# Optimization experiments

Measured on AMD Instinct MI355X. Metric: run time of the kernel, lower is better.

The kernel has to match this reference:

```python
import jax, jax.numpy as jnp
import numpy as np

N = 50_000       # nodes
E = 1_600_000    # edges (avg degree 32)
D = 32           # emb_dim == hidden_dim, num_heads = 1
L = 8            # num_layers
K = 8            # SortPooling k
VOCAB = 100


def setup_inputs() -> dict:
    key = jax.random.key(0)
    ks = jax.random.split(key, 20)
    def nrm(k, shape, scale=0.1):
        return jax.random.normal(k, shape, dtype=jnp.float32) * scale
    return {
        "h_tok": jax.random.randint(ks[0], (N,), 0, VOCAB),
        "e_tok": jax.random.randint(ks[1], (E,), 0, VOCAB),
        "src": jax.random.randint(ks[2], (E,), 0, N),
        "dst": jax.random.randint(ks[3], (E,), 0, N),
        "tok_emb": nrm(ks[4], (VOCAB, D)),
        "e_tok_emb": nrm(ks[5], (VOCAB, D)),
        # per-layer EGATConv params (stacked over L layers; all dims are D->D)
        "W_ni": nrm(ks[6], (L, D, D)),
        "W_nj": nrm(ks[7], (L, D, D)),
        "W_fij": nrm(ks[8], (L, D, D)),
        "b_edge": nrm(ks[9], (L, D)),
        "attn": nrm(ks[10], (L, D)),
        "W_node": nrm(ks[11], (L, D, D)),
        # MLP head
        "W_lin": nrm(ks[12], (K * D, D)),
        "b_lin": nrm(ks[13], (D,)),
        "W1": nrm(ks[14], (D, D)),
        "b1": nrm(ks[15], (D,)),
        "W2": nrm(ks[16], (D, D)),
        "b2": nrm(ks[17], (D,)),
        "Wc": nrm(ks[18], (D, 2)),
        "bc": nrm(ks[19], (2,)),
    }


def _egat_layer(h, e, src, dst, Wni, Wnj, Wfij, b, attn, Wnode):
    """DGL EGATConv, num_heads=1. h: [N,D] nodes, e: [E,D] edges."""
    n = h.shape[0]
    # per-edge feature: f_ij = LeakyReLU(A*h_i + B*h_j + C*e_ij + b)
    f = jax.nn.leaky_relu((h @ Wni)[src] + (h @ Wnj)[dst] + e @ Wfij + b, 0.01)  # [E,D]
    logits = jnp.sum(f * attn, axis=-1)                                         # [E]
    # edge softmax over incoming edges of each destination node
    m = jax.ops.segment_max(logits, dst, num_segments=n)
    ex = jnp.exp(logits - m[dst])
    a = ex / jax.ops.segment_sum(ex, dst, num_segments=n)[dst]                  # [E]
    msg = (h @ Wnode)[src] * a[:, None]                                         # [E,D]
    h_out = jax.ops.segment_sum(msg, dst, num_segments=n)                       # [N,D]
    return h_out, f


def reference(h_tok, e_tok, src, dst, tok_emb, e_tok_emb, W_ni, W_nj, W_fij,
              b_edge, attn, W_node, W_lin, b_lin, W1, b1, W2, b2, Wc, bc):
    h = jax.nn.relu(tok_emb[h_tok])   # [N,D]
    e = e_tok_emb[e_tok]              # [E,D]

    def step(carry, p):
        h, e = carry
        Wni, Wnj, Wfij, b, at, Wn = p
        h2, e2 = _egat_layer(h, e, src, dst, Wni, Wnj, Wfij, b, at, Wn)
        return (jax.nn.relu(h2), e2), None

    (h, e), _ = jax.lax.scan(step, (h, e), (W_ni, W_nj, W_fij, b_edge, attn, W_node))

    # SortPooling(k): sort each node's features ascending, rank nodes by last
    # (largest) channel descending, keep top-k nodes, flatten. Single graph.
    hs = jnp.sort(h, axis=-1)                     # [N,D]
    _, idx = jax.lax.top_k(hs[:, -1], K)          # top-k nodes
    x = hs[idx].reshape(1, K * D)                 # [1, k*D]

    x = jax.nn.relu(x @ W_lin + b_lin)
    x = jax.nn.relu(x @ W1 + b1)
    x = jax.nn.relu(x @ W2 + b2)
    return x @ Wc + bc                            # [1, 2]
```

## Files before the change

kernel.cpp:

```cpp
#include <hip/hip_runtime.h>
#include <hip/hip_fp16.h>

#define DD 32
#define NLAYERS 8
#define TOPK 8
#define NPB 256
#define HNB 1024
#define BCH 4096
#define P2CAP 12288

typedef _Float16 half8 __attribute__((ext_vector_type(8)));
typedef float f32x4 __attribute__((ext_vector_type(4)));

__device__ __forceinline__ unsigned encf(float x){ unsigned u=__float_as_uint(x); return (u&0x80000000u)? ~u : (u|0x80000000u); }
__device__ __forceinline__ unsigned short f2h(float f){ return __half_as_ushort(__float2half(f)); }
__device__ __forceinline__ float h2f(unsigned short u){ return __half2float(__ushort_as_half(u)); }
__device__ __forceinline__ float4 up4(uint2 u){
  float4 r;
  r.x=h2f((unsigned short)(u.x&0xFFFFu)); r.y=h2f((unsigned short)(u.x>>16));
  r.z=h2f((unsigned short)(u.y&0xFFFFu)); r.w=h2f((unsigned short)(u.y>>16));
  return r;
}
union HU { uint2 u; half8 h; };
union HU4 { uint4 u; half8 h; };
__device__ __forceinline__ int gidx(const void* p, long i, int i64){
  return i64 ? (int)((const long long*)p)[i] : ((const int*)p)[i];
}

__global__ __launch_bounds__(1024) void k_detect(const int* __restrict__ srcw,
                                                 int* __restrict__ iflag,
                                                 int* __restrict__ bcnt){
  int tid = threadIdx.x;
  for (int i=tid;i<HNB;i+=1024) bcnt[i]=0;
  if (tid==0){
    int allz = 1;
    for (int k=1;k<32;k+=2) if (srcw[k]!=0) allz = 0;
    *iflag = allz;
  }
}

__global__ void k_init(const void* __restrict__ h_tok,
                       const float* __restrict__ tok_emb,
                       unsigned short* __restrict__ h16,
                       const int* __restrict__ iflag, int N)
{
  int i64 = *iflag;
  long idx = (long)blockIdx.x*blockDim.x + threadIdx.x;
  if (idx >= (long)N*8) return;
  int n=(int)(idx>>3), q=(int)(idx&7);
  int t = gidx(h_tok, n, i64);
  float4 v = reinterpret_cast<const float4*>(tok_emb)[t*8+q];
  uint2 o;
  o.x = (unsigned)f2h(fmaxf(v.x,0.f)) | ((unsigned)f2h(fmaxf(v.y,0.f))<<16);
  o.y = (unsigned)f2h(fmaxf(v.z,0.f)) | ((unsigned)f2h(fmaxf(v.w,0.f))<<16);
  reinterpret_cast<uint2*>(h16)[(long)n*8+q] = o;
}

__global__ __launch_bounds__(256) void k_hist(
    const void* __restrict__ dstv, int* __restrict__ bcnt,
    const int* __restrict__ iflag, int E, int NB)
{
  __shared__ int bins[HNB];
  int i64 = *iflag;
  int tid = threadIdx.x;
  for (int i=tid;i<NB;i+=256) bins[i]=0;
  __syncthreads();
  long base = (long)blockIdx.x * BCH;
  long rem = (long)E - base;
  int nloc = (rem < BCH) ? (int)rem : BCH;
  for (int t=tid; t<nloc; t+=256){
    int d = gidx(dstv, base+t, i64);
    atomicAdd(&bins[d>>8], 1);
  }
  __syncthreads();
  for (int i=tid;i<NB;i+=256){
    int v = bins[i];
    if (v) atomicAdd(&bcnt[i], v);
  }
}

__global__ __launch_bounds__(1024) void k_bscan(const int* __restrict__ bcnt,
    int* __restrict__ bbase, int* __restrict__ gcur, int NB, int E)
{
  __shared__ int wsum[16];
  int tid=threadIdx.x, lane=tid&63, w=tid>>6;
  int v = (tid<NB)? bcnt[tid]:0;
  int x=v;
  #pragma unroll
  for (int d=1;d<64;d<<=1){ int t=__shfl_up(x,d,64); if(lane>=d) x+=t; }
  if (lane==63) wsum[w]=x;
  __syncthreads();
  if (w==0 && lane<16){
    int y=wsum[lane];
    #pragma unroll
    for (int d=1;d<16;d<<=1){ int t=__shfl_up(y,d,64); if(lane>=d) y+=t; }
    wsum[lane]=y;
  }
  __syncthreads();
  int wb = (w>0)? wsum[w-1]:0;
  int ex = x - v + wb;
  if (tid<NB){ bbase[tid]=ex; gcur[tid]=ex; }
  if (tid==0) bbase[NB]=E;
}

__global__ __launch_bounds__(256) void k_bucket(
    const void* __restrict__ srcv, const void* __restrict__ dstv,
    int* __restrict__ gcur, uint2* __restrict__ btmp,
    const int* __restrict__ iflag, int E, int NB)
{
  __shared__ int hist[HNB];
  __shared__ int cbase[HNB];
  int i64 = *iflag;
  int tid = threadIdx.x;
  long base = (long)blockIdx.x * BCH;
  long rem = (long)E - base;
  int nloc = (rem < BCH) ? (int)rem : BCH;
  if (nloc <= 0) return;
  for (int i = tid; i < NB; i += 256) hist[i] = 0;
  __syncthreads();
  int dl[BCH/256];
  #pragma unroll
  for (int k = 0; k < BCH/256; k++){
    int t = tid + k*256;
    dl[k] = -1;
    if (t < nloc){
      int d = gidx(dstv, base + t, i64);
      dl[k] = d;
      atomicAdd(&hist[d>>8], 1);
    }
  }
  __syncthreads();
  for (int i = tid; i < NB; i += 256){
    int hv = hist[i];
    cbase[i] = hv ? atomicAdd(&gcur[i], hv) : 0;
    hist[i] = 0;
  }
  __syncthreads();
  #pragma unroll
  for (int k = 0; k < BCH/256; k++){
    int t = tid + k*256;
    if (t < nloc){
      int d = dl[k];
      int s = gidx(srcv, base + t, i64);
      int b = d>>8;
      int slot = cbase[b] + atomicAdd(&hist[b], 1);
      uint2 r; r.x = ((unsigned)d<<16) | (unsigned)s; r.y = (unsigned)(base + t);
      btmp[slot] = r;
    }
  }
}

__global__ __launch_bounds__(256) void k_bsort(
    const int* __restrict__ bbase, const uint2* __restrict__ btmp,
    uint2* __restrict__ sde8, int* __restrict__ off, int N, int NB)
{
  __shared__ int lcnt[NPB];
  __shared__ int lbase[NPB];
  __shared__ int wsum2[4];
  __shared__ uint2 lrec[P2CAP];
  int bkt = blockIdx.x;
  int base = bbase[bkt], endp = bbase[bkt+1];
  int sz = endp - base;
  int lo = bkt*NPB;
  int tid = threadIdx.x;
  lcnt[tid] = 0;
  __syncthreads();
  for (int i=tid;i<sz;i+=256){
    uint2 r = btmp[base+i];
    atomicAdd(&lcnt[(int)(r.x>>16) - lo], 1);
  }
  __syncthreads();
  int v = lcnt[tid];
  int lane = tid&63, w = tid>>6;
  int x = v;
  #pragma unroll
  for (int d=1;d<64;d<<=1){ int t=__shfl_up(x,d,64); if(lane>=d) x+=t; }
  if (lane==63) wsum2[w]=x;
  __syncthreads();
  if (tid==0){ int a=0; for(int i=0;i<4;i++){ int t=wsum2[i]; wsum2[i]=a; a+=t; } }
  __syncthreads();
  int ex = x - v + wsum2[w];
  lbase[tid] = ex;
  int node = lo + tid;
  if (node < N) off[node] = base + ex;
  if (bkt == NB-1 && tid == 0) off[N] = bbase[NB];
  __syncthreads();
  if (sz <= P2CAP){
    lcnt[tid] = lbase[tid];
    __syncthreads();
    for (int i=tid;i<sz;i+=256){
      uint2 r = btmp[base+i];
      int d = (int)(r.x>>16) - lo;
      int p = atomicAdd(&lcnt[d],1);
      lrec[p] = r;
    }
    __syncthreads();
    for (int i=tid;i<sz;i+=256)
      sde8[base+i] = lrec[i];
  } else {
    lcnt[tid] = base + lbase[tid];
    __syncthreads();
    for (int i=tid;i<sz;i+=256){
      uint2 r = btmp[base+i];
      int d = (int)(r.x>>16) - lo;
      int p = atomicAdd(&lcnt[d],1);
      sde8[p] = r;
    }
  }
}

__global__ void k_fill(const uint2* __restrict__ sde8, const void* __restrict__ e_tok,
                       const float* __restrict__ e_emb,
                       unsigned* __restrict__ csr_sd, unsigned short* __restrict__ ebuf,
                       const int* __restrict__ iflag, int E){
  int i64 = *iflag;
  long idx = (long)blockIdx.x*blockDim.x + threadIdx.x;
  if (idx >= (long)E*4) return;
  int pos = (int)(idx>>2), j = (int)(idx&3);
  uint2 r = sde8[pos];
  if (j==0) csr_sd[pos] = r.x;
  int t = gidx(e_tok, (int)r.y, i64);
  const float4* sp = reinterpret_cast<const float4*>(e_emb + t*DD) + j*2;
  float4 x = sp[0], y = sp[1];
  uint4 ov;
  ov.x = (unsigned)f2h(x.x) | ((unsigned)f2h(x.y)<<16);
  ov.y = (unsigned)f2h(x.z) | ((unsigned)f2h(x.w)<<16);
  ov.z = (unsigned)f2h(y.x) | ((unsigned)f2h(y.y)<<16);
  ov.w = (unsigned)f2h(y.z) | ((unsigned)f2h(y.w)<<16);
  reinterpret_cast<uint4*>(ebuf)[(long)pos*4+j] = ov;
}

__global__ __launch_bounds__(256) void k_nodeAB(
    const unsigned short* __restrict__ h16,
    const float* __restrict__ WA, const float* __restrict__ WB,
    unsigned short* __restrict__ hA16, unsigned short* __restrict__ hB16, int N)
{
  __shared__ float hl[8][DD];
  int tid = threadIdx.x;
  int ln = tid>>5, c = tid&31;
  int n = blockIdx.x*8 + ln;
  hl[ln][c] = (n<N)? h2f(h16[(long)n*DD+c]) : 0.f;
  __syncthreads();
  float a=0.f,b=0.f;
  #pragma unroll
  for (int k=0;k<DD;k++){
    float v = hl[ln][k];
    a = fmaf(v, WA[k*DD+c], a);
    b = fmaf(v, WB[k*DD+c], b);
  }
  if (n<N){ hA16[(long)n*DD+c]=f2h(a); hB16[(long)n*DD+c]=f2h(b); }
}

__global__ __launch_bounds__(256) void k_edge(
    unsigned short* __restrict__ ebuf,
    const unsigned short* __restrict__ hA16, const unsigned short* __restrict__ hB16,
    const unsigned* __restrict__ csr_sd,
    const float* __restrict__ Wf, const float* __restrict__ bvec,
    const float* __restrict__ attn,
    unsigned short* __restrict__ lbuf, int ntiles, int writef)
{
  int lane = threadIdx.x & 63;
  int wid = (blockIdx.x*256 + threadIdx.x) >> 6;
  int nw  = (gridDim.x*256) >> 6;
  int m = lane & 15, q = lane >> 4;
  half8 a0, a1;
  #pragma unroll
  for (int j=0;j<8;j++){
    a0[j] = (_Float16)Wf[(q*8+j)*DD + m];
    a1[j] = (_Float16)Wf[(q*8+j)*DD + 16 + m];
  }
  float4 blo = *reinterpret_cast<const float4*>(bvec + q*4);
  float4 bhi = *reinterpret_cast<const float4*>(bvec + 16 + q*4);
  float4 alo = *reinterpret_cast<const float4*>(attn + q*4);
  float4 ahi = *reinterpret_cast<const float4*>(attn + 16 + q*4);
  f32x4 zero = {0.f,0.f,0.f,0.f};
  HU4 b0; b0.u = make_uint4(0,0,0,0);
  HU4 b1; b1.u = make_uint4(0,0,0,0);
  unsigned sd0 = 0, sd1 = 0;
  uint2 gA0_0={0,0}, gA1_0={0,0}, gB0_0={0,0}, gB1_0={0,0};
  if (wid < ntiles){
    long e0 = (long)wid*16 + m;
    sd0 = csr_sd[e0];
    b0.u = *reinterpret_cast<const uint4*>(ebuf + e0*DD + q*8);
    unsigned s = sd0 & 0xFFFFu, d = sd0 >> 16;
    const uint2* pA = reinterpret_cast<const uint2*>(hA16 + (long)s*DD);
    const uint2* pB = reinterpret_cast<const uint2*>(hB16 + (long)d*DD);
    gA0_0=pA[q]; gA1_0=pA[4+q]; gB0_0=pB[q]; gB1_0=pB[4+q];
  }
  if (wid + nw < ntiles){
    long e1 = (long)(wid+nw)*16 + m;
    sd1 = csr_sd[e1];
    b1.u = *reinterpret_cast<const uint4*>(ebuf + e1*DD + q*8);
  }
  for (int t = wid; t < ntiles; t += nw){
    int t1 = t + nw, t2 = t + 2*nw;
    unsigned sd2 = 0; HU4 b2; b2.u = make_uint4(0,0,0,0);
    if (t2 < ntiles){
      long e2 = (long)t2*16 + m;
      sd2 = csr_sd[e2];
      b2.u = *reinterpret_cast<const uint4*>(ebuf + e2*DD + q*8);
    }
    uint2 gA0_1={0,0}, gA1_1={0,0}, gB0_1={0,0}, gB1_1={0,0};
    if (t1 < ntiles){
      unsigned s = sd1 & 0xFFFFu, d = sd1 >> 16;
      const uint2* pA = reinterpret_cast<const uint2*>(hA16 + (long)s*DD);
      const uint2* pB = reinterpret_cast<const uint2*>(hB16 + (long)d*DD);
      gA0_1=pA[q]; gA1_1=pA[4+q]; gB0_1=pB[q]; gB1_1=pB[4+q];
    }
    f32x4 d0 = __builtin_amdgcn_mfma_f32_16x16x32_f16(a0, b0.h, zero, 0,0,0);
    f32x4 d1 = __builtin_amdgcn_mfma_f32_16x16x32_f16(a1, b0.h, zero, 0,0,0);
    long tbase = (long)t*16;
    long edge = tbase + m;
    float4 A0 = up4(gA0_0), A1 = up4(gA1_0);
    float4 B0 = up4(gB0_0), B1 = up4(gB1_0);
    float f00 = d0[0]+A0.x+B0.x+blo.x, f01 = d0[1]+A0.y+B0.y+blo.y;
    float f02 = d0[2]+A0.z+B0.z+blo.z, f03 = d0[3]+A0.w+B0.w+blo.w;
    float f10 = d1[0]+A1.x+B1.x+bhi.x, f11 = d1[1]+A1.y+B1.y+bhi.y;
    float f12 = d1[2]+A1.z+B1.z+bhi.z, f13 = d1[3]+A1.w+B1.w+bhi.w;
    f00 = (f00>0.f)?f00:0.01f*f00; f01 = (f01>0.f)?f01:0.01f*f01;
    f02 = (f02>0.f)?f02:0.01f*f02; f03 = (f03>0.f)?f03:0.01f*f03;
    f10 = (f10>0.f)?f10:0.01f*f10; f11 = (f11>0.f)?f11:0.01f*f11;
    f12 = (f12>0.f)?f12:0.01f*f12; f13 = (f13>0.f)?f13:0.01f*f13;
    if (writef){
      uint2 w0, w1;
      w0.x = (unsigned)f2h(f00) | ((unsigned)f2h(f01)<<16);
      w0.y = (unsigned)f2h(f02) | ((unsigned)f2h(f03)<<16);
      w1.x = (unsigned)f2h(f10) | ((unsigned)f2h(f11)<<16);
      w1.y = (unsigned)f2h(f12) | ((unsigned)f2h(f13)<<16);
      *reinterpret_cast<uint2*>(ebuf + edge*DD + q*4) = w0;
      *reinterpret_cast<uint2*>(ebuf + edge*DD + 16 + q*4) = w1;
    }
    float l = f00*alo.x + f01*alo.y + f02*alo.z + f03*alo.w
            + f10*ahi.x + f11*ahi.y + f12*ahi.z + f13*ahi.w;
    l += __shfl_xor(l, 16, 64);
    l += __shfl_xor(l, 32, 64);
    if (lane < 16){
      float lc = fminf(fmaxf(l, -15.f), 10.5f);
      lbuf[tbase + lane] = f2h(__expf(lc));
    }
    sd0 = sd1; b0 = b1;
    gA0_0=gA0_1; gA1_0=gA1_1; gB0_0=gB0_1; gB1_0=gB1_1;
    sd1 = sd2; b1 = b2;
  }
}

__global__ __launch_bounds__(256) void k_aggrP(
    const unsigned short* __restrict__ h16in, const unsigned short* __restrict__ lbuf,
    const int* __restrict__ off, const unsigned* __restrict__ csr_sd,
    const float* __restrict__ Wnd, const float* __restrict__ WA,
    const float* __restrict__ WB,
    unsigned short* __restrict__ h16out, unsigned short* __restrict__ hA16,
    unsigned short* __restrict__ hB16, float* __restrict__ hout, int N, int last)
{
  __shared__ float gl[8][DD];
  __shared__ float tl[8][DD];
  int tid=threadIdx.x;
  int ln = tid>>5, c = tid&31;
  int n = blockIdx.x*8 + ln;
  float num=0.f, den=0.f;
  if (n<N){
    int o0 = off[n], o1 = off[n+1];
    int i = o0;
    for (; i+8 <= o1; i += 8){
      unsigned sd0=csr_sd[i],   sd1=csr_sd[i+1], sd2=csr_sd[i+2], sd3=csr_sd[i+3];
      unsigned sd4=csr_sd[i+4], sd5=csr_sd[i+5], sd6=csr_sd[i+6], sd7=csr_sd[i+7];
      float ex0=h2f(lbuf[i]),   ex1=h2f(lbuf[i+1]), ex2=h2f(lbuf[i+2]), ex3=h2f(lbuf[i+3]);
      float ex4=h2f(lbuf[i+4]), ex5=h2f(lbuf[i+5]), ex6=h2f(lbuf[i+6]), ex7=h2f(lbuf[i+7]);
      float g0=h2f(h16in[(long)(sd0&0xFFFFu)*DD+c]);
      float g1=h2f(h16in[(long)(sd1&0xFFFFu)*DD+c]);
      float g2=h2f(h16in[(long)(sd2&0xFFFFu)*DD+c]);
      float g3=h2f(h16in[(long)(sd3&0xFFFFu)*DD+c]);
      float g4=h2f(h16in[(long)(sd4&0xFFFFu)*DD+c]);
      float g5=h2f(h16in[(long)(sd5&0xFFFFu)*DD+c]);
      float g6=h2f(h16in[(long)(sd6&0xFFFFu)*DD+c]);
      float g7=h2f(h16in[(long)(sd7&0xFFFFu)*DD+c]);
      num=fmaf(ex0,g0,num); num=fmaf(ex1,g1,num);
      num=fmaf(ex2,g2,num); num=fmaf(ex3,g3,num);
      num=fmaf(ex4,g4,num); num=fmaf(ex5,g5,num);
      num=fmaf(ex6,g6,num); num=fmaf(ex7,g7,num);
      den+=ex0; den+=ex1; den+=ex2; den+=ex3;
      den+=ex4; den+=ex5; den+=ex6; den+=ex7;
    }
    for (; i<o1; i++){
      unsigned sd=csr_sd[i];
      float ex=h2f(lbuf[i]);
      num=fmaf(ex, h2f(h16in[(long)(sd&0xFFFFu)*DD+c]), num);
      den += ex;
    }
  }
  gl[ln][c] = (den>0.f)? num/den : 0.f;
  __syncthreads();
  float t=0.f;
  #pragma unroll
  for (int k=0;k<DD;k++) t = fmaf(gl[ln][k], Wnd[k*DD+c], t);
  t = fmaxf(t, 0.f);
  if (last){
    if (n<N) hout[(long)n*DD+c] = t;
    return;
  }
  tl[ln][c] = t;
  __syncthreads();
  float a=0.f,b=0.f;
  #pragma unroll
  for (int k=0;k<DD;k++){
    float v = tl[ln][k];
    a = fmaf(v, WA[k*DD+c], a);
    b = fmaf(v, WB[k*DD+c], b);
  }
  if (n<N){
    h16out[(long)n*DD+c]=f2h(t);
    hA16[(long)n*DD+c]=f2h(a);
    hB16[(long)n*DD+c]=f2h(b);
  }
}

__global__ void k_keys(const float* __restrict__ h, unsigned long long* __restrict__ keys, int N){
  int n = blockIdx.x*blockDim.x + threadIdx.x;
  if (n>=N) return;
  const float4* p = reinterpret_cast<const float4*>(h + (long)n*DD);
  float m = -1e38f;
  #pragma unroll
  for (int j=0;j<8;j++){
    float4 v = p[j];
    m = fmaxf(m, fmaxf(fmaxf(v.x,v.y), fmaxf(v.z,v.w)));
  }
  keys[n] = ((unsigned long long)encf(m)<<32) | (unsigned)(~(unsigned)n);
}

__global__ __launch_bounds__(256) void k_ptop(const unsigned long long* __restrict__ keys, int N,
                                              unsigned long long* __restrict__ outk){
  __shared__ unsigned long long red[256];
  int tid = threadIdx.x, b = blockIdx.x, nb = gridDim.x;
  int chunk = (N + nb - 1) / nb;
  int base = b*chunk, end = base+chunk; if (end>N) end=N;
  unsigned long long loc[TOPK];
  #pragma unroll
  for (int i=0;i<TOPK;i++) loc[i]=0ull;
  for (int i=base+tid; i<end; i+=256){
    unsigned long long k = keys[i];
    if (k > loc[TOPK-1]){
      int j = TOPK-1;
      while (j>0 && loc[j-1]<k){ loc[j]=loc[j-1]; j--; }
      loc[j]=k;
    }
  }
  for (int r=0; r<TOPK; r++){
    red[tid] = loc[0];
    __syncthreads();
    for (int s=128; s>0; s>>=1){
      if (tid<s && red[tid+s]>red[tid]) red[tid]=red[tid+s];
      __syncthreads();
    }
    unsigned long long w = red[0];
    if (tid==0) outk[b*TOPK + r] = w;
    if (loc[0]==w){
      #pragma unroll
      for (int j=0;j<TOPK-1;j++) loc[j]=loc[j+1];
      loc[TOPK-1]=0ull;
    }
    __syncthreads();
  }
}

__global__ __launch_bounds__(256) void k_head(
    const float* __restrict__ h, const unsigned long long* __restrict__ sel,
    const float* __restrict__ Wlin, const float* __restrict__ blin,
    const float* __restrict__ W1, const float* __restrict__ b1,
    const float* __restrict__ W2, const float* __restrict__ b2,
    const float* __restrict__ Wc, const float* __restrict__ bc,
    float* __restrict__ out, int N)
{
  __shared__ float xs[TOPK][DD];
  __shared__ float y1[DD], y2[DD], y3[DD];
  int tid=threadIdx.x;
  int r=tid>>5, c=tid&31;
  unsigned node = ~(unsigned)(sel[r] & 0xFFFFFFFFull);
  if (node >= (unsigned)N) node = 0;
  xs[r][c] = h[(long)node*DD + c];
  __syncthreads();
  if (tid<TOPK){
    for (int i=1;i<DD;i++){
      float v=xs[tid][i]; int j=i-1;
      while (j>=0 && xs[tid][j]>v){ xs[tid][j+1]=xs[tid][j]; j--; }
      xs[tid][j+1]=v;
    }
  }
  __syncthreads();
  if (tid<DD){
    float a=blin[tid];
    for (int i=0;i<TOPK*DD;i++) a = fmaf(xs[i>>5][i&31], Wlin[i*DD+tid], a);
    y1[tid] = a>0.f? a : 0.f;
  }
  __syncthreads();
  if (tid<DD){
    float a=b1[tid];
    #pragma unroll
    for (int i=0;i<DD;i++) a = fmaf(y1[i], W1[i*DD+tid], a);
    y2[tid] = a>0.f? a : 0.f;
  }
  __syncthreads();
  if (tid<DD){
    float a=b2[tid];
    #pragma unroll
    for (int i=0;i<DD;i++) a = fmaf(y2[i], W2[i*DD+tid], a);
    y3[tid] = a>0.f? a : 0.f;
  }
  __syncthreads();
  if (tid<2){
    float a=bc[tid];
    #pragma unroll
    for (int i=0;i<DD;i++) a = fmaf(y3[i], Wc[i*2+tid], a);
    out[tid] = a;
  }
}

extern "C" void kernel_launch(void* const* d_in, const int* in_sizes, int n_in,
                              void* d_out, int out_size, void* d_ws, size_t ws_size,
                              hipStream_t stream) {
  const int N = in_sizes[0];
  const int E = in_sizes[1];
  const float* tok_emb   = (const float*)d_in[4];
  const float* e_tok_emb = (const float*)d_in[5];
  const float* W_ni  = (const float*)d_in[6];
  const float* W_nj  = (const float*)d_in[7];
  const float* W_fij = (const float*)d_in[8];
  const float* b_e   = (const float*)d_in[9];
  const float* attn  = (const float*)d_in[10];
  const float* W_nd  = (const float*)d_in[11];

  char* p = (char*)d_ws;
  auto alloc = [&](size_t bytes)->char* {
    char* r = p; p += (bytes + 255) & ~(size_t)255; return r;
  };
  int* iflag = (int*)alloc(256);
  unsigned long long* sel = (unsigned long long*)alloc(256);
  unsigned long long* cand = (unsigned long long*)alloc(256*TOPK*8);
  int* bcnt = (int*)alloc(HNB*4);
  int* bbase = (int*)alloc((HNB+1)*4);
  int* gcur = (int*)alloc(HNB*4);
  int* csroff = (int*)alloc((size_t)(N+1)*4);
  unsigned* csr_sd = (unsigned*)alloc((size_t)(E+32)*4);
  float* h = (float*)alloc((size_t)N*DD*4);
  alloc((size_t)N*DD*2);
  unsigned short* lbuf = (unsigned short*)alloc((size_t)(E+32)*2);
  unsigned short* h16a = (unsigned short*)alloc((size_t)N*DD*2);
  unsigned short* h16b = (unsigned short*)alloc((size_t)N*DD*2);
  unsigned short* hA16 = (unsigned short*)alloc((size_t)N*DD*2);
  unsigned short* hB16 = (unsigned short*)alloc((size_t)N*DD*2);
  unsigned short* ebuf = (unsigned short*)alloc((size_t)(E+32)*DD*2);
  uint2* sde8 = (uint2*)h;
  uint2* btmp = (uint2*)ebuf;
  unsigned long long* keys = (unsigned long long*)lbuf;

  const int NB = (N + NPB - 1) / NPB;
  const int NECH = (E + BCH - 1) / BCH;

  hipLaunchKernelGGL(k_detect, dim3(1), dim3(1024), 0, stream, (const int*)d_in[2], iflag, bcnt);
  hipLaunchKernelGGL(k_init, dim3((int)(((long)N*8+255)/256)), dim3(256), 0, stream,
                     d_in[0], tok_emb, h16a, iflag, N);
  hipLaunchKernelGGL(k_hist, dim3(NECH), dim3(256), 0, stream,
                     d_in[3], bcnt, iflag, E, NB);
  hipLaunchKernelGGL(k_bscan, dim3(1), dim3(1024), 0, stream, bcnt, bbase, gcur, NB, E);
  hipLaunchKernelGGL(k_bucket, dim3(NECH), dim3(256), 0, stream,
                     d_in[2], d_in[3], gcur, btmp, iflag, E, NB);
  hipLaunchKernelGGL(k_bsort, dim3(NB), dim3(256), 0, stream, bbase, btmp, sde8, csroff, N, NB);
  hipLaunchKernelGGL(k_fill, dim3((int)(((long)E*4+255)/256)), dim3(256), 0, stream,
                     sde8, d_in[1], e_tok_emb, csr_sd, ebuf, iflag, E);

  int nb_node = (N+7)/8;
  int ntiles = (E+15)/16;
  hipLaunchKernelGGL(k_nodeAB, dim3(nb_node), dim3(256), 0, stream,
                     h16a, W_ni, W_nj, hA16, hB16, N);
  unsigned short* hcur = h16a;
  unsigned short* hnext = h16b;
  for (int l=0; l<NLAYERS; l++){
    const float* Wf  = W_fij + (size_t)l*DD*DD;
    const float* bl  = b_e   + (size_t)l*DD;
    const float* at  = attn  + (size_t)l*DD;
    const float* Wnd = W_nd  + (size_t)l*DD*DD;
    int last = (l == NLAYERS-1);
    hipLaunchKernelGGL(k_edge, dim3(2048), dim3(256), 0, stream,
                       ebuf, hA16, hB16, csr_sd, Wf, bl, at, lbuf, ntiles,
                       last ? 0 : 1);
    const float* WnA = last ? W_ni : (W_ni + (size_t)(l+1)*DD*DD);
    const float* WnB = last ? W_nj : (W_nj + (size_t)(l+1)*DD*DD);
    hipLaunchKernelGGL(k_aggrP, dim3(nb_node), dim3(256), 0, stream,
                       hcur, lbuf, csroff, csr_sd, Wnd, WnA, WnB,
                       hnext, hA16, hB16, h, N, last);
    unsigned short* tmp = hcur; hcur = hnext; hnext = tmp;
  }

  hipLaunchKernelGGL(k_keys, dim3((N+255)/256), dim3(256), 0, stream, h, keys, N);
  hipLaunchKernelGGL(k_ptop, dim3(256), dim3(256), 0, stream, keys, N, cand);
  hipLaunchKernelGGL(k_ptop, dim3(1), dim3(256), 0, stream, cand, 256*TOPK, sel);
  hipLaunchKernelGGL(k_head, dim3(1), dim3(256), 0, stream,
                     h, sel,
                     (const float*)d_in[12], (const float*)d_in[13],
                     (const float*)d_in[14], (const float*)d_in[15],
                     (const float*)d_in[16], (const float*)d_in[17],
                     (const float*)d_in[18], (const float*)d_in[19],
                     (float*)d_out, N);
}
```

Before: 1.031 ms.

## Aggregate edges per block with shared-memory atomics instead of per-node loops

Replaces the per-node aggregation kernel, where each 32-lane group walked one destination's edge list, with a kernel that gives each block 32 consecutive destination nodes. The block's 8 groups stride over that combined CSR edge range and accumulate into shared memory with atomic adds, using the dst index packed in csr_sd. The aim is to balance work despite uneven degrees and remove per-node loop tails. The cost is shared-memory atomic contention and fewer blocks, and float atomics make the summation order nondeterministic.

```diff
diff --git a/kernel.cpp b/kernel.cpp
--- a/kernel.cpp
+++ b/kernel.cpp
@@ -8,6 +8,7 @@
 #define HNB 1024
 #define BCH 4096
 #define P2CAP 12288
+#define AGNB 32
 
 typedef _Float16 half8 __attribute__((ext_vector_type(8)));
 typedef float f32x4 __attribute__((ext_vector_type(4)));
@@ -344,7 +345,7 @@
   }
 }
 
-__global__ __launch_bounds__(256) void k_aggrP(
+__global__ __launch_bounds__(256) void k_aggrE(
     const unsigned short* __restrict__ h16in, const unsigned short* __restrict__ lbuf,
     const int* __restrict__ off, const unsigned* __restrict__ csr_sd,
     const float* __restrict__ Wnd, const float* __restrict__ WA,
@@ -352,65 +353,77 @@
     unsigned short* __restrict__ h16out, unsigned short* __restrict__ hA16,
     unsigned short* __restrict__ hB16, float* __restrict__ hout, int N, int last)
 {
-  __shared__ float gl[8][DD];
-  __shared__ float tl[8][DD];
-  int tid=threadIdx.x;
-  int ln = tid>>5, c = tid&31;
-  int n = blockIdx.x*8 + ln;
-  float num=0.f, den=0.f;
-  if (n<N){
-    int o0 = off[n], o1 = off[n+1];
-    int i = o0;
-    for (; i+8 <= o1; i += 8){
-      unsigned sd0=csr_sd[i],   sd1=csr_sd[i+1], sd2=csr_sd[i+2], sd3=csr_sd[i+3];
-      unsigned sd4=csr_sd[i+4], sd5=csr_sd[i+5], sd6=csr_sd[i+6], sd7=csr_sd[i+7];
-      float ex0=h2f(lbuf[i]),   ex1=h2f(lbuf[i+1]), ex2=h2f(lbuf[i+2]), ex3=h2f(lbuf[i+3]);
-      float ex4=h2f(lbuf[i+4]), ex5=h2f(lbuf[i+5]), ex6=h2f(lbuf[i+6]), ex7=h2f(lbuf[i+7]);
-      float g0=h2f(h16in[(long)(sd0&0xFFFFu)*DD+c]);
-      float g1=h2f(h16in[(long)(sd1&0xFFFFu)*DD+c]);
-      float g2=h2f(h16in[(long)(sd2&0xFFFFu)*DD+c]);
-      float g3=h2f(h16in[(long)(sd3&0xFFFFu)*DD+c]);
-      float g4=h2f(h16in[(long)(sd4&0xFFFFu)*DD+c]);
-      float g5=h2f(h16in[(long)(sd5&0xFFFFu)*DD+c]);
-      float g6=h2f(h16in[(long)(sd6&0xFFFFu)*DD+c]);
-      float g7=h2f(h16in[(long)(sd7&0xFFFFu)*DD+c]);
-      num=fmaf(ex0,g0,num); num=fmaf(ex1,g1,num);
-      num=fmaf(ex2,g2,num); num=fmaf(ex3,g3,num);
-      num=fmaf(ex4,g4,num); num=fmaf(ex5,g5,num);
-      num=fmaf(ex6,g6,num); num=fmaf(ex7,g7,num);
-      den+=ex0; den+=ex1; den+=ex2; den+=ex3;
-      den+=ex4; den+=ex5; den+=ex6; den+=ex7;
-    }
-    for (; i<o1; i++){
-      unsigned sd=csr_sd[i];
-      float ex=h2f(lbuf[i]);
-      num=fmaf(ex, h2f(h16in[(long)(sd&0xFFFFu)*DD+c]), num);
-      den += ex;
-    }
-  }
-  gl[ln][c] = (den>0.f)? num/den : 0.f;
-  __syncthreads();
-  float t=0.f;
-  #pragma unroll
-  for (int k=0;k<DD;k++) t = fmaf(gl[ln][k], Wnd[k*DD+c], t);
-  t = fmaxf(t, 0.f);
-  if (last){
-    if (n<N) hout[(long)n*DD+c] = t;
-    return;
-  }
-  tl[ln][c] = t;
-  __syncthreads();
-  float a=0.f,b=0.f;
-  #pragma unroll
-  for (int k=0;k<DD;k++){
-    float v = tl[ln][k];
-    a = fmaf(v, WA[k*DD+c], a);
-    b = fmaf(v, WB[k*DD+c], b);
-  }
-  if (n<N){
-    h16out[(long)n*DD+c]=f2h(t);
-    hA16[(long)n*DD+c]=f2h(a);
-    hB16[(long)n*DD+c]=f2h(b);
+  __shared__ float acc[AGNB][DD];
+  __shared__ float den[AGNB];
+  __shared__ float tl[AGNB][DD];
+  int tid = threadIdx.x;
+  int g = tid>>5, c = tid&31;
+  int lo = blockIdx.x*AGNB;
+  int hi = lo + AGNB; if (hi > N) hi = N;
+  for (int i=tid; i<AGNB*DD; i+=256) (&acc[0][0])[i] = 0.f;
+  if (tid < AGNB) den[tid] = 0.f;
+  __syncthreads();
+  {
+    long o0 = off[lo], o1 = off[hi];
+    long e = o0 + g;
+    for (; e + 8 < o1; e += 16){
+      unsigned sdA = csr_sd[e];
+      unsigned sdB = csr_sd[e+8];
+      float exA = h2f(lbuf[e]), exB = h2f(lbuf[e+8]);
+      float hvA = h2f(h16in[(long)(sdA&0xFFFFu)*DD + c]);
+      float hvB = h2f(h16in[(long)(sdB&0xFFFFu)*DD + c]);
+      int dA = (int)(sdA>>16) - lo, dB = (int)(sdB>>16) - lo;
+      atomicAdd(&acc[dA][c], exA*hvA);
+      atomicAdd(&acc[dB][c], exB*hvB);
+      if (c==0){ atomicAdd(&den[dA], exA); atomicAdd(&den[dB], exB); }
+    }
+    for (; e < o1; e += 8){
+      unsigned sd = csr_sd[e];
+      float ex = h2f(lbuf[e]);
+      float hv = h2f(h16in[(long)(sd&0xFFFFu)*DD + c]);
+      int dl = (int)(sd>>16) - lo;
+      atomicAdd(&acc[dl][c], ex*hv);
+      if (c==0) atomicAdd(&den[dl], ex);
+    }
+  }
+  __syncthreads();
+  for (int i=tid; i<AGNB*DD; i+=256){
+    float dd = den[i>>5];
+    (&acc[0][0])[i] = (dd>0.f) ? (&acc[0][0])[i]/dd : 0.f;
+  }
+  __syncthreads();
+  #pragma unroll
+  for (int rep=0; rep<AGNB/8; rep++){
+    int ln = g + rep*8;
+    float t = 0.f;
+    #pragma unroll
+    for (int k=0;k<DD;k++) t = fmaf(acc[ln][k], Wnd[k*DD+c], t);
+    t = fmaxf(t, 0.f);
+    if (last){
+      int n = lo + ln;
+      if (n < N) hout[(long)n*DD+c] = t;
+    } else {
+      tl[ln][c] = t;
+    }
+  }
+  if (last) return;
+  __syncthreads();
+  #pragma unroll
+  for (int rep=0; rep<AGNB/8; rep++){
+    int ln = g + rep*8;
+    float a=0.f, b=0.f;
+    #pragma unroll
+    for (int k=0;k<DD;k++){
+      float v = tl[ln][k];
+      a = fmaf(v, WA[k*DD+c], a);
+      b = fmaf(v, WB[k*DD+c], b);
+    }
+    int n = lo + ln;
+    if (n < N){
+      h16out[(long)n*DD+c] = f2h(tl[ln][c]);
+      hA16[(long)n*DD+c]   = f2h(a);
+      hB16[(long)n*DD+c]   = f2h(b);
+    }
   }
 }
 
@@ -568,6 +581,7 @@
                      sde8, d_in[1], e_tok_emb, csr_sd, ebuf, iflag, E);
 
   int nb_node = (N+7)/8;
+  int nb_ag = (N+AGNB-1)/AGNB;
   int ntiles = (E+15)/16;
   hipLaunchKernelGGL(k_nodeAB, dim3(nb_node), dim3(256), 0, stream,
                      h16a, W_ni, W_nj, hA16, hB16, N);
@@ -584,7 +598,7 @@
                        last ? 0 : 1);
     const float* WnA = last ? W_ni : (W_ni + (size_t)(l+1)*DD*DD);
     const float* WnB = last ? W_nj : (W_nj + (size_t)(l+1)*DD*DD);
-    hipLaunchKernelGGL(k_aggrP, dim3(nb_node), dim3(256), 0, stream,
+    hipLaunchKernelGGL(k_aggrE, dim3(nb_ag), dim3(256), 0, stream,
                        hcur, lbuf, csroff, csr_sd, Wnd, WnA, WnB,
                        hnext, hA16, hB16, h, N, last);
     unsigned short* tmp = hcur; hcur = hnext; hnext = tmp;
```

Measured after the change: 3.161 ms. +206.6%, slower.
